# Kernel optimization log

Hardware: AMD Instinct MI355X
Metric: run time of the kernel (lower is better)

The kernel has to match this reference:

```python
import jax, jax.numpy as jnp
import numpy as np

N_ATOM = 30000
N_PAIR = 1_000_000
N_TRI = 4_000_000
N_SF = 16
RC = 6.0

LAMBD = jnp.array([-1.0, 1.0] * 8, dtype=jnp.float32)
ZETA = jnp.array([1.0, 1.0, 2.0, 2.0, 4.0, 4.0, 8.0, 8.0] * 2, dtype=jnp.float32)
ETA = jnp.array([0.01, 0.014, 0.02, 0.028, 0.04, 0.056, 0.08, 0.11,
                 0.16, 0.22, 0.32, 0.45, 0.63, 0.72, 0.9, 1.0], dtype=jnp.float32)


def cutoff_f1(r):
    # PiNN 'f1' cutoff: 0.5*(cos(pi*r/rc)+1)
    return 0.5 * (jnp.cos(jnp.float32(np.pi) * r / RC) + 1.0)


def gaussian_basis(r, fc):
    # GaussianBasis with center=0, gamma=eta: fc * exp(-eta * r^2), shape [n, n_sf]
    return fc[:, None] * jnp.exp(-ETA[None, :] * (r[:, None] ** 2))


def setup_inputs() -> dict:
    key = jax.random.key(0)
    k1, k2, k3, k4, k5 = jax.random.split(key, 5)
    ind_2 = jax.random.randint(k1, (N_PAIR, 2), 0, N_ATOM, dtype=jnp.int32)
    ind_3 = jax.random.randint(k2, (N_TRI, 2), 0, N_PAIR, dtype=jnp.int32)
    dist = jax.random.uniform(k3, (N_PAIR,), jnp.float32, 0.5, RC)
    dirs = jax.random.normal(k4, (N_PAIR, 3), jnp.float32)
    dirs = dirs / jnp.linalg.norm(dirs, axis=1, keepdims=True)
    diff = dirs * dist[:, None]  # bond vectors consistent with dist
    elems = jax.random.randint(k5, (N_ATOM,), 0, 4, dtype=jnp.int32)
    fc = cutoff_f1(dist)
    return {"ind_2": ind_2, "ind_3": ind_3, "dist": dist, "diff": diff,
            "elems": elems, "fc": fc}


def reference(ind_2, ind_3, dist, diff, elems, fc):
    # i=j=k='ALL': species filter is identity; a_rind = arange(n_atom)
    ind_ij = ind_3[:, 0]
    ind_ik = ind_3[:, 1]
    i_rind = ind_2[ind_ij, 0]  # central atom index per triplet

    diff_ij = diff[ind_ij]  # [T,3]
    diff_ik = diff[ind_ik]
    diff_jk = diff_ik - diff_ij
    dist_jk = jnp.linalg.norm(diff_jk, axis=1)
    mask = dist_jk < RC  # TF filters triplets; we mask (jit-friendly)

    fc_jk = cutoff_f1(dist_jk)
    dist_ij = dist[ind_ij]
    dist_ik = dist[ind_ik]
    fc_ij = fc[ind_ij]
    fc_ik = fc[ind_ik]

    cos_ijk = jnp.einsum('id,id->i', diff_ij, diff_ik) / dist_ij / dist_ik
    base = jnp.maximum(1.0 + LAMBD[None, :] * cos_ijk[:, None], 0.0)
    sf = (2.0 ** (1.0 - ZETA[None, :]) * base ** ZETA[None, :]
          * gaussian_basis(dist_ij, fc_ij)
          * gaussian_basis(dist_ik, fc_ik)
          * gaussian_basis(dist_jk, fc_jk))
    sf = jnp.where(mask[:, None], sf, 0.0)

    # scatter_nd add into per-atom fingerprints
    fp = jnp.zeros((N_ATOM, N_SF), dtype=sf.dtype).at[i_rind].add(sf)

    # jacobian indices: central-atom rel index per participating pair
    vals = jnp.where(mask, i_rind, -1)
    seg = jnp.concatenate([ind_ij, ind_ik])
    pair_i = jax.ops.segment_max(jnp.concatenate([vals, vals]), seg,
                                 num_segments=N_PAIR)
    pair_i = jnp.maximum(pair_i, -1)  # empty segments -> -1 sentinel
    jacob_ind = jnp.stack([jnp.arange(N_PAIR, dtype=jnp.int32), pair_i], axis=1)
    return fp, jacob_ind
```

## Files before the change

### kernel.cpp

```cpp
#include <hip/hip_runtime.h>

#define N_ATOM 30000
#define N_PAIR 1000000
#define N_TRI  4000000
#define N_SF   16
#define FP_ELEMS (N_ATOM * N_SF)

#define ASH  5
#define APB  32
#define NCB  938
#define NSUB 8
#define NSEG (NCB * NSUB)
#define OVF_CNT_IDX NSEG
#define OVF_CAP 131072
#define TILE 4096
#define PER_TH 16
#define NTILES ((N_TRI + TILE - 1) / TILE)

#define OFF_CCNT  0ULL
#define OFF_IKMAX 65536ULL
#define OFF_AOFP  4065536ULL
#define OFF_FLAG  6065536ULL
#define OFF_OVF   7065536ULL
#define OFF_PACK  8114112ULL
#define OFF_CB    24114112ULL

__device__ __constant__ float c_eta[16] = {
    0.01f, 0.014f, 0.02f, 0.028f, 0.04f, 0.056f, 0.08f, 0.11f,
    0.16f, 0.22f, 0.32f, 0.45f, 0.63f, 0.72f, 0.9f, 1.0f};

__device__ __forceinline__ bool tri_math_pack(
    float4 A, float4 B, float A8[8], float& R2)
{
    float ax = A.x, ay = A.y, az = A.z, fcij = A.w;
    float bx = B.x, by = B.y, bz = B.z, fcik = B.w;
    float d2ij = fmaf(ax, ax, fmaf(ay, ay, az * az));
    float d2ik = fmaf(bx, bx, fmaf(by, by, bz * bz));
    float jx = bx - ax, jy = by - ay, jz = bz - az;
    float d2jk = fmaf(jx, jx, fmaf(jy, jy, jz * jz));
    if (!(d2jk < 36.0f)) return false;
    float dij = sqrtf(d2ij);
    float dik = sqrtf(d2ik);
    float djk = sqrtf(d2jk);
    const float PI_OVER_RC = 0.5235987755982988f;
    float fcjk = 0.5f * (__cosf(PI_OVER_RC * djk) + 1.0f);
    float dot = fmaf(ax, bx, fmaf(ay, by, az * bz));
    float cosv = dot / (dij * dik);
    R2 = d2ij + d2ik + d2jk;
    float FCt = fcij * fcik * fcjk;
    float bm = fmaxf(1.0f - cosv, 0.0f);
    float bp = fmaxf(1.0f + cosv, 0.0f);
    float bm2 = bm * bm, bp2 = bp * bp;
    float bm4 = bm2 * bm2, bp4 = bp2 * bp2;
    float bm8 = bm4 * bm4, bp8 = bp4 * bp4;
    A8[0] = FCt * bm;              A8[1] = FCt * bp;
    A8[2] = 0.5f * FCt * bm2;      A8[3] = 0.5f * FCt * bp2;
    A8[4] = 0.125f * FCt * bm4;    A8[5] = 0.125f * FCt * bp4;
    A8[6] = 0.0078125f * FCt * bm8; A8[7] = 0.0078125f * FCt * bp8;
    return true;
}


__global__ __launch_bounds__(256) void prep2(
    const int2* __restrict__ ind2, const float* __restrict__ diff,
    const float* __restrict__ fc,
    int* __restrict__ ccnt, int* __restrict__ ikmax,
    unsigned short* __restrict__ aofp, unsigned char* __restrict__ flag,
    float4* __restrict__ pack)
{
    int p = blockIdx.x * blockDim.x + threadIdx.x;
    if (p <= NSEG) ccnt[p] = 0;
    if (p >= N_PAIR) return;
    ikmax[p] = -1;
    flag[p] = 0;
    aofp[p] = (unsigned short)ind2[p].x;
    float4 r;
    r.x = diff[3 * p + 0];
    r.y = diff[3 * p + 1];
    r.z = diff[3 * p + 2];
    r.w = fc[p];
    pack[p] = r;
}

__global__ __launch_bounds__(256) void bin3(
    const int2* __restrict__ ind3, const unsigned short* __restrict__ aofp,
    int* __restrict__ ccnt, int2* __restrict__ cbucket,
    int2* __restrict__ ovf, int cap)
{
    __shared__ int lcnt[NCB];
    __shared__ int lbase[NCB];
    const int thr = threadIdx.x;
    const int sub = blockIdx.x & (NSUB - 1);
    const long long t0 = (long long)blockIdx.x * TILE;

    for (int i = thr; i < NCB; i += 256) lcnt[i] = 0;
    __syncthreads();

    int myatom[PER_TH];
    int myslot[PER_TH];
#pragma unroll
    for (int j = 0; j < PER_TH; ++j) {
        long long t = t0 + j * 256 + thr;
        int a = 0, s = -1;
        if (t < N_TRI) {
            int ij = ind3[t].x;
            a = aofp[ij];
            s = atomicAdd(&lcnt[a >> ASH], 1);
        }
        myatom[j] = a;
        myslot[j] = s;
    }
    __syncthreads();
    for (int c = thr; c < NCB; c += 256) {
        int n = lcnt[c];
        lbase[c] = n ? atomicAdd(&ccnt[c * NSUB + sub], n) : 0;
    }
    __syncthreads();
#pragma unroll
    for (int j = 0; j < PER_TH; ++j) {
        long long t = t0 + j * 256 + thr;
        if (t >= N_TRI) continue;
        int a = myatom[j];
        int c = a >> ASH;
        int slot = lbase[c] + myslot[j];
        int2 pr = ind3[t];
        if (slot < cap) {
            int2 e;
            e.x = pr.x | ((a & (APB - 1)) << 20);
            e.y = pr.y;
            cbucket[(size_t)(c * NSUB + sub) * cap + slot] = e;
        } else {
            int o = atomicAdd(&ccnt[OVF_CNT_IDX], 1);
            if (o < OVF_CAP) ovf[o] = pr;
        }
    }
}

__global__ __launch_bounds__(256) void reduce3(
    const int* __restrict__ ccnt, const int2* __restrict__ cbucket, int cap,
    const float4* __restrict__ pack,
    int* __restrict__ ikmax, unsigned char* __restrict__ flag,
    float* __restrict__ out)
{
    __shared__ float lacc[APB * 17];
    const int b = blockIdx.x;
    const int thr = threadIdx.x;
    for (int i = thr; i < APB * 17; i += 256) lacc[i] = 0.0f;
    __syncthreads();

    for (int sub = 0; sub < NSUB; ++sub) {
        int n = ccnt[b * NSUB + sub];
        n = min(n, cap);
        const int2* seg = cbucket + (size_t)(b * NSUB + sub) * cap;
        for (int i = thr; i < n; i += 256) {
            int2 e = seg[i];
            int a5 = (e.x >> 20) & (APB - 1);
            int ij = e.x & 0xFFFFF;
            int ik = e.y;
            float4 A = pack[ij];
            float4 B = pack[ik];
            float A8[8], R2;
            if (!tri_math_pack(A, B, A8, R2)) continue;
            flag[ij] = 1;
            atomicMax(&ikmax[ik], (b << ASH) + a5);
#pragma unroll
            for (int s = 0; s < 16; ++s)
                atomicAdd(&lacc[a5 * 17 + s], A8[s & 7] * __expf(-c_eta[s] * R2));
        }
    }
    __syncthreads();
    for (int t = thr; t < APB * N_SF; t += 256) {
        int atom = (b << ASH) + (t >> 4);
        if (atom < N_ATOM)
            out[(size_t)atom * N_SF + (t & 15)] = lacc[(t >> 4) * 17 + (t & 15)];
    }
}

__global__ __launch_bounds__(256) void ovf3(
    const int* __restrict__ ccnt, const int2* __restrict__ ovf,
    const float4* __restrict__ pack, const unsigned short* __restrict__ aofp,
    int* __restrict__ ikmax, unsigned char* __restrict__ flag,
    float* __restrict__ out)
{
    int i = blockIdx.x * blockDim.x + threadIdx.x;
    int n = ccnt[OVF_CNT_IDX];
    if (n > OVF_CAP) n = OVF_CAP;
    if (i >= n) return;
    int2 pr = ovf[i];
    int ij = pr.x, ik = pr.y;
    float A8[8], R2;
    if (!tri_math_pack(pack[ij], pack[ik], A8, R2)) return;
    int atom = aofp[ij];
    flag[ij] = 1;
    atomicMax(&ikmax[ik], atom);
    float* base = out + (size_t)atom * N_SF;
#pragma unroll
    for (int s = 0; s < 16; ++s)
        unsafeAtomicAdd(base + s, A8[s & 7] * __expf(-c_eta[s] * R2));
}

__global__ __launch_bounds__(256) void fin3(
    const int* __restrict__ ikmax, const unsigned char* __restrict__ flag,
    const unsigned short* __restrict__ aofp, float* __restrict__ out)
{
    int p = blockIdx.x * blockDim.x + threadIdx.x;
    if (p >= N_PAIR) return;
    int v = ikmax[p];
    if (flag[p]) { int a = aofp[p]; v = v > a ? v : a; }
    float* jf = out + FP_ELEMS;
    jf[2 * p + 0] = (float)p;
    jf[2 * p + 1] = (float)v;
}


__device__ __forceinline__ bool tri_math_raw(
    int ij, int ik, const float* dist, const float* diff, const float* fc,
    float A8[8], float& R2)
{
    float4 A, B;
    A.x = diff[3 * ij + 0]; A.y = diff[3 * ij + 1]; A.z = diff[3 * ij + 2]; A.w = fc[ij];
    B.x = diff[3 * ik + 0]; B.y = diff[3 * ik + 1]; B.z = diff[3 * ik + 2]; B.w = fc[ik];
    return tri_math_pack(A, B, A8, R2);
}

__global__ __launch_bounds__(256) void init_legacy(float* __restrict__ out) {
    int i = blockIdx.x * blockDim.x + threadIdx.x;
    if (i < FP_ELEMS) out[i] = 0.0f;
    if (i < N_PAIR) ((int*)out + FP_ELEMS)[2 * i + 1] = -1;
}

__global__ __launch_bounds__(256) void tri_legacy(
    const int* __restrict__ ind2, const int2* __restrict__ ind3,
    const float* __restrict__ dist, const float* __restrict__ diff,
    const float* __restrict__ fc, float* __restrict__ out) {
    int t = blockIdx.x * blockDim.x + threadIdx.x;
    if (t >= N_TRI) return;
    int2 pr = ind3[t];
    int ij = pr.x, ik = pr.y;
    float A8[8], R2;
    if (!tri_math_raw(ij, ik, dist, diff, fc, A8, R2)) return;
    int atom = ind2[2 * ij];
    int* jac = (int*)out + FP_ELEMS;
    atomicMax(&jac[2 * ij + 1], atom);
    atomicMax(&jac[2 * ik + 1], atom);
    float* base = out + (size_t)atom * N_SF;
#pragma unroll
    for (int s = 0; s < 16; ++s)
        unsafeAtomicAdd(base + s, A8[s & 7] * __expf(-c_eta[s] * R2));
}

__global__ __launch_bounds__(256) void fin_legacy(float* __restrict__ out) {
    int p = blockIdx.x * blockDim.x + threadIdx.x;
    if (p >= N_PAIR) return;
    int* jac = (int*)out + FP_ELEMS;
    int v = jac[2 * p + 1];
    float* jf = (float*)jac;
    jf[2 * p + 0] = (float)p;
    jf[2 * p + 1] = (float)v;
}


extern "C" void kernel_launch(void* const* d_in, const int* in_sizes, int n_in,
                              void* d_out, int out_size, void* d_ws, size_t ws_size,
                              hipStream_t stream) {
    const int2*  ind2 = (const int2*)d_in[0];
    const int2*  ind3 = (const int2*)d_in[1];
    const float* dist = (const float*)d_in[2];
    const float* diff = (const float*)d_in[3];
    const float* fc   = (const float*)d_in[5];
    float* out = (float*)d_out;

    const size_t seg_stride = (size_t)NSEG * sizeof(int2);
    const size_t need_min = OFF_CB + seg_stride * 608;

    if (ws_size >= need_min) {
        char* ws = (char*)d_ws;
        int* ccnt            = (int*)(ws + OFF_CCNT);
        int* ikmax           = (int*)(ws + OFF_IKMAX);
        unsigned short* aofp = (unsigned short*)(ws + OFF_AOFP);
        unsigned char* flag  = (unsigned char*)(ws + OFF_FLAG);
        int2* ovf            = (int2*)(ws + OFF_OVF);
        float4* pack         = (float4*)(ws + OFF_PACK);
        int2* cbucket        = (int2*)(ws + OFF_CB);
        int cap = (int)((ws_size - OFF_CB) / seg_stride);
        if (cap > 1024) cap = 1024;

        int pb = (N_PAIR + 255) / 256;
        prep2<<<pb, 256, 0, stream>>>(ind2, diff, fc, ccnt, ikmax, aofp, flag, pack);
        bin3<<<NTILES, 256, 0, stream>>>(ind3, aofp, ccnt, cbucket, ovf, cap);
        reduce3<<<NCB, 256, 0, stream>>>(ccnt, cbucket, cap, pack, ikmax, flag, out);
        ovf3<<<OVF_CAP / 256, 256, 0, stream>>>(ccnt, ovf, pack, aofp, ikmax, flag, out);
        fin3<<<pb, 256, 0, stream>>>(ikmax, flag, aofp, out);
    } else {
        init_legacy<<<(N_PAIR + 255) / 256, 256, 0, stream>>>(out);
        tri_legacy<<<(N_TRI + 255) / 256, 256, 0, stream>>>((const int*)d_in[0], ind3, dist, diff, fc, out);
        fin_legacy<<<(N_PAIR + 255) / 256, 256, 0, stream>>>(out);
    }
}
```

Measured before the change: 458.5 us.

## Split reduce into one block per sub-bucket with atomic flush to output

The reduce kernel now launches one block per (atom-chunk, sub-bucket) segment, 8x more blocks than before, instead of one block looping over all eight sub-buckets. The aim is more parallelism and better load balance across the GPU. Because several blocks now contribute to the same atoms, each block flushes its shared accumulator to global memory with atomic adds, and the prep kernel zeroes the fingerprint output first. The cost is extra global atomics, an extra zeroing pass, and repeated shared-memory initialization per block.

```diff
diff --git a/kernel.cpp b/kernel.cpp
--- a/kernel.cpp
+++ b/kernel.cpp
@@ -66,10 +66,11 @@
     const float* __restrict__ fc,
     int* __restrict__ ccnt, int* __restrict__ ikmax,
     unsigned short* __restrict__ aofp, unsigned char* __restrict__ flag,
-    float4* __restrict__ pack)
+    float4* __restrict__ pack, float* __restrict__ out)
 {
     int p = blockIdx.x * blockDim.x + threadIdx.x;
     if (p <= NSEG) ccnt[p] = 0;
+    if (p < FP_ELEMS) out[p] = 0.0f;
     if (p >= N_PAIR) return;
     ikmax[p] = -1;
     flag[p] = 0;
@@ -136,43 +137,43 @@
     }
 }
 
-__global__ __launch_bounds__(256) void reduce3(
+__global__ __launch_bounds__(256) void reduce4(
     const int* __restrict__ ccnt, const int2* __restrict__ cbucket, int cap,
     const float4* __restrict__ pack,
     int* __restrict__ ikmax, unsigned char* __restrict__ flag,
     float* __restrict__ out)
 {
     __shared__ float lacc[APB * 17];
-    const int b = blockIdx.x;
+    const int seg = blockIdx.x;
+    const int b = seg >> 3;
     const int thr = threadIdx.x;
     for (int i = thr; i < APB * 17; i += 256) lacc[i] = 0.0f;
     __syncthreads();
 
-    for (int sub = 0; sub < NSUB; ++sub) {
-        int n = ccnt[b * NSUB + sub];
-        n = min(n, cap);
-        const int2* seg = cbucket + (size_t)(b * NSUB + sub) * cap;
-        for (int i = thr; i < n; i += 256) {
-            int2 e = seg[i];
-            int a5 = (e.x >> 20) & (APB - 1);
-            int ij = e.x & 0xFFFFF;
-            int ik = e.y;
-            float4 A = pack[ij];
-            float4 B = pack[ik];
-            float A8[8], R2;
-            if (!tri_math_pack(A, B, A8, R2)) continue;
-            flag[ij] = 1;
-            atomicMax(&ikmax[ik], (b << ASH) + a5);
-#pragma unroll
-            for (int s = 0; s < 16; ++s)
-                atomicAdd(&lacc[a5 * 17 + s], A8[s & 7] * __expf(-c_eta[s] * R2));
-        }
+    int n = ccnt[seg];
+    n = min(n, cap);
+    const int2* segp = cbucket + (size_t)seg * cap;
+    for (int i = thr; i < n; i += 256) {
+        int2 e = segp[i];
+        int a5 = (e.x >> 20) & (APB - 1);
+        int ij = e.x & 0xFFFFF;
+        int ik = e.y;
+        float4 A = pack[ij];
+        float4 B = pack[ik];
+        float A8[8], R2;
+        if (!tri_math_pack(A, B, A8, R2)) continue;
+        flag[ij] = 1;
+        atomicMax(&ikmax[ik], (b << ASH) + a5);
+#pragma unroll
+        for (int s = 0; s < 16; ++s)
+            atomicAdd(&lacc[a5 * 17 + s], A8[s & 7] * __expf(-c_eta[s] * R2));
     }
     __syncthreads();
     for (int t = thr; t < APB * N_SF; t += 256) {
         int atom = (b << ASH) + (t >> 4);
-        if (atom < N_ATOM)
-            out[(size_t)atom * N_SF + (t & 15)] = lacc[(t >> 4) * 17 + (t & 15)];
+        float v = lacc[(t >> 4) * 17 + (t & 15)];
+        if (atom < N_ATOM && v != 0.0f)
+            unsafeAtomicAdd(out + (size_t)atom * N_SF + (t & 15), v);
     }
 }
 
@@ -213,16 +214,6 @@
 }
 
 
-__device__ __forceinline__ bool tri_math_raw(
-    int ij, int ik, const float* dist, const float* diff, const float* fc,
-    float A8[8], float& R2)
-{
-    float4 A, B;
-    A.x = diff[3 * ij + 0]; A.y = diff[3 * ij + 1]; A.z = diff[3 * ij + 2]; A.w = fc[ij];
-    B.x = diff[3 * ik + 0]; B.y = diff[3 * ik + 1]; B.z = diff[3 * ik + 2]; B.w = fc[ik];
-    return tri_math_pack(A, B, A8, R2);
-}
-
 __global__ __launch_bounds__(256) void init_legacy(float* __restrict__ out) {
     int i = blockIdx.x * blockDim.x + threadIdx.x;
     if (i < FP_ELEMS) out[i] = 0.0f;
@@ -237,8 +228,11 @@
     if (t >= N_TRI) return;
     int2 pr = ind3[t];
     int ij = pr.x, ik = pr.y;
+    float4 A, B;
+    A.x = diff[3 * ij + 0]; A.y = diff[3 * ij + 1]; A.z = diff[3 * ij + 2]; A.w = fc[ij];
+    B.x = diff[3 * ik + 0]; B.y = diff[3 * ik + 1]; B.z = diff[3 * ik + 2]; B.w = fc[ik];
     float A8[8], R2;
-    if (!tri_math_raw(ij, ik, dist, diff, fc, A8, R2)) return;
+    if (!tri_math_pack(A, B, A8, R2)) return;
     int atom = ind2[2 * ij];
     int* jac = (int*)out + FP_ELEMS;
     atomicMax(&jac[2 * ij + 1], atom);
@@ -286,14 +280,14 @@
         if (cap > 1024) cap = 1024;
 
         int pb = (N_PAIR + 255) / 256;
-        prep2<<<pb, 256, 0, stream>>>(ind2, diff, fc, ccnt, ikmax, aofp, flag, pack);
+        prep2<<<pb, 256, 0, stream>>>(ind2, diff, fc, ccnt, ikmax, aofp, flag, pack, out);
         bin3<<<NTILES, 256, 0, stream>>>(ind3, aofp, ccnt, cbucket, ovf, cap);
-        reduce3<<<NCB, 256, 0, stream>>>(ccnt, cbucket, cap, pack, ikmax, flag, out);
+        reduce4<<<NSEG, 256, 0, stream>>>(ccnt, cbucket, cap, pack, ikmax, flag, out);
         ovf3<<<OVF_CAP / 256, 256, 0, stream>>>(ccnt, ovf, pack, aofp, ikmax, flag, out);
         fin3<<<pb, 256, 0, stream>>>(ikmax, flag, aofp, out);
     } else {
         init_legacy<<<(N_PAIR + 255) / 256, 256, 0, stream>>>(out);
-        tri_legacy<<<(N_TRI + 255) / 256, 256, 0, stream>>>((const int*)d_in[0], ind3, dist, diff, fc, out);
+        tri_legacy<<<(N_PAIR * 4 + 255) / 256, 256, 0, stream>>>((const int*)d_in[0], ind3, dist, diff, fc, out);
         fin_legacy<<<(N_PAIR + 255) / 256, 256, 0, stream>>>(out);
     }
 }
```

Result: faster. 447.5 us (-2.4%).
